# Optimization experiments

Hardware: AMD Instinct MI355X
Metric: run time of the kernel (lower is better)

Reference implementation:

```python
import jax, jax.numpy as jnp
import numpy as np

N_NODES = 20000
N_EDGES = 400000
B = 4            # number of edge_attr tensors in the Python loop (batch of graphs)
NODE_DIM = 256   # == hidden_dim (required: forward feeds raw x into edge_fc)
EDGE_DIM = 16
HIDDEN = 256
OUT_DIM = 128


def setup_inputs() -> dict:
    key = jax.random.key(0)
    ks = jax.random.split(key, 6)
    x = jax.random.normal(ks[0], (N_NODES, NODE_DIM), dtype=jnp.float32)
    edge_index = jax.random.randint(ks[1], (2, N_EDGES), 0, N_NODES, dtype=jnp.int64)
    edge_attrs = jax.random.normal(ks[2], (B, N_EDGES, EDGE_DIM), dtype=jnp.float32)
    fan_in = 2 * HIDDEN + EDGE_DIM  # edge_fc in_features
    W_edge = jax.random.normal(ks[3], (fan_in, HIDDEN), dtype=jnp.float32) / np.sqrt(fan_in).astype(np.float32)
    b_edge = jnp.zeros((HIDDEN,), dtype=jnp.float32)
    W_graph = jax.random.normal(ks[4], (HIDDEN, OUT_DIM), dtype=jnp.float32) / np.sqrt(HIDDEN).astype(np.float32)
    b_graph = jnp.zeros((OUT_DIM,), dtype=jnp.float32)
    return {"x": x, "edge_index": edge_index, "edge_attrs": edge_attrs,
            "W_edge": W_edge, "b_edge": b_edge, "W_graph": W_graph, "b_graph": b_graph}


def reference(x, edge_index, edge_attrs, W_edge, b_edge, W_graph, b_graph):
    # Original: for each edge_attr in edge_attrs:
    #   relu(cat([x[src], x[dst], edge_attr]) @ W_edge + b).mean(0) @ W_graph + b_graph
    # Equivalent: split W_edge by the concat blocks; the (src,dst) contribution is
    # shared across the batch, so compute it once and broadcast.
    D = x.shape[1]
    W_src, W_dst, W_attr = W_edge[:D], W_edge[D:2 * D], W_edge[2 * D:]
    src = x[edge_index[0]]                      # [E, D] gather
    dst = x[edge_index[1]]                      # [E, D] gather
    base = src @ W_src + dst @ W_dst + b_edge   # [E, H]
    h = jax.nn.relu(base[None, :, :] + jnp.einsum('bea,ah->beh', edge_attrs, W_attr))  # [B, E, H]
    graph_feat = h.mean(axis=1)                 # [B, H] mean pool over edges
    return graph_feat @ W_graph + b_graph       # [B, OUT]
```

## Files before the change

kernel.cpp:

```cpp
#include <hip/hip_runtime.h>

#define N_NODES 20000
#define N_EDGES 400000
#define NODE_DIM 256
#define HIDDEN 256
#define OUT_DIM 128
#define PROJ_BLOCKS 628
#define CONV_BLOCKS 256

typedef __attribute__((ext_vector_type(8))) short short8;
typedef __attribute__((ext_vector_type(4))) float f32x4;

__device__ inline unsigned short f2bf(float f) {
  union { float f; unsigned u; } v; v.f = f;
  unsigned r = (v.u + 0x7FFFu + ((v.u >> 16) & 1u)) >> 16;
  return (unsigned short)r;
}

__global__ __launch_bounds__(256) void proj_mfma(
    const float* __restrict__ x, const float* __restrict__ We,
    const float* __restrict__ be, unsigned short* __restrict__ C,
    float* __restrict__ partial, const float* __restrict__ attrs,
    unsigned short* __restrict__ attrs_bf) {
  const int tid = threadIdx.x;
  if (blockIdx.x >= PROJ_BLOCKS) {
    const int nt = CONV_BLOCKS * 256;
    const int total4 = 4 * N_EDGES * 16 / 4;
    for (int i = (blockIdx.x - PROJ_BLOCKS) * 256 + tid; i < total4; i += nt) {
      float4 v = ((const float4*)attrs)[i];
      ushort4 o;
      o.x = f2bf(v.x); o.y = f2bf(v.y); o.z = f2bf(v.z); o.w = f2bf(v.w);
      ((ushort4*)attrs_bf)[i] = o;
    }
    return;
  }
  if (blockIdx.x == 0) {
    for (int i = tid; i < 4 * HIDDEN; i += 256) partial[i] = 0.f;
  }
  const int bm = blockIdx.x >> 2;
  const int bn = blockIdx.x & 3;
  const int row0 = bm * 128;
  const int col0 = bn * 128;
  const int half = col0 >> 8;
  const int ncol0 = col0 & 255;
  const int lane = tid & 63, wave = tid >> 6;
  const int q = lane >> 4, c = lane & 15;
  const int wm = wave >> 1, wn = wave & 1;

  __shared__ unsigned short As[128][32];
  __shared__ unsigned short Bs[128][32];

  f32x4 acc[4][4];
#pragma unroll
  for (int i = 0; i < 4; ++i)
#pragma unroll
    for (int t = 0; t < 4; ++t) acc[i][t] = (f32x4){0.f, 0.f, 0.f, 0.f};

  const int ar = tid >> 1;
  const int ak = (tid & 1) * 16;
  const int bk = tid >> 3;
  const int bn0 = (tid & 7) * 16;

  for (int k0 = 0; k0 < NODE_DIM; k0 += 32) {
    {
      const int r = row0 + ar;
      short8 t0, t1;
      if (r < N_NODES) {
        const float4* src = (const float4*)&x[(size_t)r * NODE_DIM + k0 + ak];
        float4 f0 = src[0], f1 = src[1], f2 = src[2], f3 = src[3];
        t0[0]=f2bf(f0.x); t0[1]=f2bf(f0.y); t0[2]=f2bf(f0.z); t0[3]=f2bf(f0.w);
        t0[4]=f2bf(f1.x); t0[5]=f2bf(f1.y); t0[6]=f2bf(f1.z); t0[7]=f2bf(f1.w);
        t1[0]=f2bf(f2.x); t1[1]=f2bf(f2.y); t1[2]=f2bf(f2.z); t1[3]=f2bf(f2.w);
        t1[4]=f2bf(f3.x); t1[5]=f2bf(f3.y); t1[6]=f2bf(f3.z); t1[7]=f2bf(f3.w);
      } else {
#pragma unroll
        for (int j = 0; j < 8; ++j) { t0[j] = 0; t1[j] = 0; }
      }
      *(short8*)&As[ar][ak] = t0;
      *(short8*)&As[ar][ak + 8] = t1;
    }
    {
      const float4* src = (const float4*)&We[(size_t)(half * 256 + k0 + bk) * HIDDEN + ncol0 + bn0];
#pragma unroll
      for (int v = 0; v < 4; ++v) {
        float4 f = src[v];
        Bs[bn0 + v * 4 + 0][bk] = f2bf(f.x);
        Bs[bn0 + v * 4 + 1][bk] = f2bf(f.y);
        Bs[bn0 + v * 4 + 2][bk] = f2bf(f.z);
        Bs[bn0 + v * 4 + 3][bk] = f2bf(f.w);
      }
    }
    __syncthreads();
    short8 Af[4], Bf[4];
#pragma unroll
    for (int i = 0; i < 4; ++i) Af[i] = *(const short8*)&As[wm * 64 + i * 16 + c][q * 8];
#pragma unroll
    for (int t = 0; t < 4; ++t) Bf[t] = *(const short8*)&Bs[wn * 64 + t * 16 + c][q * 8];
#pragma unroll
    for (int i = 0; i < 4; ++i)
#pragma unroll
      for (int t = 0; t < 4; ++t)
        acc[i][t] = __builtin_amdgcn_mfma_f32_16x16x32_bf16(Af[i], Bf[t], acc[i][t], 0, 0, 0);
    __syncthreads();
  }

  float biasv[4] = {0.f, 0.f, 0.f, 0.f};
  const int nbase = ncol0 + wn * 64;
  if (half) {
#pragma unroll
    for (int t = 0; t < 4; ++t) biasv[t] = be[nbase + t * 16 + c];
  }
#pragma unroll
  for (int i = 0; i < 4; ++i) {
#pragma unroll
    for (int r = 0; r < 4; ++r) {
      const int node = row0 + wm * 64 + i * 16 + q * 4 + r;
      if (node < N_NODES) {
        ushort4 o;
        o.x = f2bf(acc[i][0][r] + biasv[0]);
        o.y = f2bf(acc[i][1][r] + biasv[1]);
        o.z = f2bf(acc[i][2][r] + biasv[2]);
        o.w = f2bf(acc[i][3][r] + biasv[3]);
        *(ushort4*)&C[(size_t)node * 512 + half * 256 + nbase + c * 4] = o;
      }
    }
  }
}

template <bool PRE>
__global__ __launch_bounds__(256) void edge_mfma(
    const unsigned short* __restrict__ C, const int* __restrict__ ei,
    const float* __restrict__ attrs_f, const unsigned short* __restrict__ attrs_b,
    const float* __restrict__ We, float* __restrict__ partial) {
  const int tid = threadIdx.x;
  const int lane = tid & 63, wave = tid >> 6;
  const int q = lane >> 4, c = lane & 15;
  const int hb = wave * 64;

  short8 Bf[4];
#pragma unroll
  for (int t = 0; t < 4; ++t) {
    short8 bf;
#pragma unroll
    for (int j = 0; j < 8; ++j) {
      int k = q * 8 + j;
      float w = (k < 16) ? We[(size_t)(512 + k) * HIDDEN + hb + t * 16 + c] : 0.0f;
      bf[j] = (short)f2bf(w);
    }
    Bf[t] = bf;
  }

  f32x4 acc4[4][4];
#pragma unroll
  for (int b = 0; b < 4; ++b)
#pragma unroll
    for (int t = 0; t < 4; ++t) acc4[b][t] = (f32x4){0.f, 0.f, 0.f, 0.f};

  const f32x4 zero4 = {0.f, 0.f, 0.f, 0.f};
  const int ngroups = N_EDGES / 16;
  for (int g = blockIdx.x; g < ngroups; g += gridDim.x) {
    const int e0 = g * 16;
    const int4 ns4 = *(const int4*)&ei[e0 + q * 4];
    const int4 nd4 = *(const int4*)&ei[N_EDGES + e0 + q * 4];

    short8 Af[4];
    if (PRE) {
      if (q < 2) {
#pragma unroll
        for (int b = 0; b < 4; ++b)
          Af[b] = *(const short8*)&attrs_b[((size_t)b * N_EDGES + e0 + c) * 16 + q * 8];
      } else {
        short8 z;
#pragma unroll
        for (int j = 0; j < 8; ++j) z[j] = 0;
#pragma unroll
        for (int b = 0; b < 4; ++b) Af[b] = z;
      }
    } else {
      if (q < 2) {
#pragma unroll
        for (int b = 0; b < 4; ++b) {
          const size_t off = ((size_t)b * N_EDGES + e0 + c) * 16 + q * 8;
          const float4 a0 = *(const float4*)&attrs_f[off];
          const float4 a1 = *(const float4*)&attrs_f[off + 4];
          short8 af;
          af[0]=f2bf(a0.x); af[1]=f2bf(a0.y); af[2]=f2bf(a0.z); af[3]=f2bf(a0.w);
          af[4]=f2bf(a1.x); af[5]=f2bf(a1.y); af[6]=f2bf(a1.z); af[7]=f2bf(a1.w);
          Af[b] = af;
        }
      } else {
        short8 z;
#pragma unroll
        for (int j = 0; j < 8; ++j) z[j] = 0;
#pragma unroll
        for (int b = 0; b < 4; ++b) Af[b] = z;
      }
    }

    f32x4 base4[4];
    {
      const int nn[4] = {ns4.x, ns4.y, ns4.z, ns4.w};
      const int dd[4] = {nd4.x, nd4.y, nd4.z, nd4.w};
#pragma unroll
      for (int r = 0; r < 4; ++r) {
        const uint2 s = *(const uint2*)&C[(size_t)nn[r] * 512 + hb + c * 4];
        const uint2 d = *(const uint2*)&C[(size_t)dd[r] * 512 + 256 + hb + c * 4];
        base4[0][r] = __uint_as_float(s.x << 16) + __uint_as_float(d.x << 16);
        base4[1][r] = __uint_as_float(s.x & 0xFFFF0000u) + __uint_as_float(d.x & 0xFFFF0000u);
        base4[2][r] = __uint_as_float(s.y << 16) + __uint_as_float(d.y << 16);
        base4[3][r] = __uint_as_float(s.y & 0xFFFF0000u) + __uint_as_float(d.y & 0xFFFF0000u);
      }
    }

#pragma unroll
    for (int b = 0; b < 4; ++b) {
#pragma unroll
      for (int t = 0; t < 4; ++t) {
        f32x4 S = __builtin_amdgcn_mfma_f32_16x16x32_bf16(Af[b], Bf[t], zero4, 0, 0, 0);
        f32x4 u = S + base4[t];
        u[0] = fmaxf(u[0], 0.f); u[1] = fmaxf(u[1], 0.f);
        u[2] = fmaxf(u[2], 0.f); u[3] = fmaxf(u[3], 0.f);
        acc4[b][t] += u;
      }
    }
  }

#pragma unroll
  for (int b = 0; b < 4; ++b)
#pragma unroll
    for (int t = 0; t < 4; ++t) {
      float v = acc4[b][t][0] + acc4[b][t][1] + acc4[b][t][2] + acc4[b][t][3];
      v += __shfl_xor(v, 16, 64);
      v += __shfl_xor(v, 32, 64);
      if (q == 0) atomicAdd(&partial[b * HIDDEN + hb + t * 16 + c], v);
    }
}

__global__ __launch_bounds__(256) void graph_out(
    const float* __restrict__ partial, const float* __restrict__ Wg,
    const float* __restrict__ bg, float* __restrict__ out) {
  const int o = blockIdx.x;
  const int hh = threadIdx.x;
  const int lane = hh & 63, wave = hh >> 6;
  const float w = Wg[(size_t)hh * OUT_DIM + o];
  float v[4];
#pragma unroll
  for (int b = 0; b < 4; ++b) v[b] = partial[b * HIDDEN + hh] * w;
#pragma unroll
  for (int off = 32; off >= 1; off >>= 1)
#pragma unroll
    for (int b = 0; b < 4; ++b) v[b] += __shfl_down(v[b], off, 64);
  __shared__ float red[4][4];
  if (lane == 0)
#pragma unroll
    for (int b = 0; b < 4; ++b) red[wave][b] = v[b];
  __syncthreads();
  if (hh < 4) {
    float s = red[0][hh] + red[1][hh] + red[2][hh] + red[3][hh];
    out[hh * OUT_DIM + o] = s * (1.0f / (float)N_EDGES) + bg[o];
  }
}

extern "C" void kernel_launch(void* const* d_in, const int* in_sizes, int n_in,
                              void* d_out, int out_size, void* d_ws, size_t ws_size,
                              hipStream_t stream) {
  const float* x  = (const float*)d_in[0];
  const int*   ei = (const int*)d_in[1];
  const float* ea = (const float*)d_in[2];
  const float* We = (const float*)d_in[3];
  const float* be = (const float*)d_in[4];
  const float* Wg = (const float*)d_in[5];
  const float* bg = (const float*)d_in[6];
  float* out = (float*)d_out;

  const size_t C_bytes = (size_t)N_NODES * 512 * 2;
  const size_t A_bytes = (size_t)4 * N_EDGES * 16 * 2;
  unsigned short* C = (unsigned short*)d_ws;
  const bool pre = ws_size >= C_bytes + A_bytes + 4096;
  unsigned short* attrs_bf = pre ? (unsigned short*)((char*)d_ws + C_bytes) : nullptr;
  float* partial = (float*)((char*)d_ws + (pre ? C_bytes + A_bytes : C_bytes));

  const int grid1 = pre ? PROJ_BLOCKS + CONV_BLOCKS : PROJ_BLOCKS;
  proj_mfma<<<grid1, 256, 0, stream>>>(x, We, be, C, partial, ea, attrs_bf);
  if (pre)
    edge_mfma<true><<<2048, 256, 0, stream>>>(C, ei, nullptr, attrs_bf, We, partial);
  else
    edge_mfma<false><<<2048, 256, 0, stream>>>(C, ei, ea, nullptr, We, partial);
  graph_out<<<128, 256, 0, stream>>>(partial, Wg, bg, out);
}
```

Measured before the change: 283.7 us.

## Restructure edge kernel around 32x32x16 MFMA with LDS-staged attrs and prefetch

The edge kernel switches from 16x16x32 MFMAs, whose K dimension was half zero-padded, to 32x32x16 MFMAs that use the weight slice as the A operand and the projected base as the accumulator input. To make the gathered row slice line up with the MFMA output layout, the projection kernel now writes columns of C in a permuted order. Attribute tiles are double-buffered into LDS with global_load_lds, and the next group's edge indices are prefetched, with the hidden dimension split across block pairs. This removes wasted MFMA work and the separate base add, and gives wider, contiguous gathers, at the cost of a barrier-based pipeline and a more complex layout coupling between the two kernels.

```diff
diff --git a/kernel.cpp b/kernel.cpp
--- a/kernel.cpp
+++ b/kernel.cpp
@@ -7,15 +7,26 @@
 #define OUT_DIM 128
 #define PROJ_BLOCKS 628
 #define CONV_BLOCKS 256
+#define EDGE_BLOCKS 2048
+#define EG 32
 
 typedef __attribute__((ext_vector_type(8))) short short8;
 typedef __attribute__((ext_vector_type(4))) float f32x4;
+typedef __attribute__((ext_vector_type(16))) float f32x16;
 
 __device__ inline unsigned short f2bf(float f) {
   union { float f; unsigned u; } v; v.f = f;
   unsigned r = (v.u + 0x7FFFu + ((v.u >> 16) & 1u)) >> 16;
   return (unsigned short)r;
 }
+
+__device__ inline void gload_lds16(const void* g, const void* l) {
+  __builtin_amdgcn_global_load_lds(
+      (const __attribute__((address_space(1))) unsigned int*)(unsigned long long)g,
+      (__attribute__((address_space(3))) unsigned int*)(unsigned int)(unsigned long long)l,
+      16, 0, 0);
+}
+
 
 __global__ __launch_bounds__(256) void proj_mfma(
     const float* __restrict__ x, const float* __restrict__ We,
@@ -84,10 +95,14 @@
 #pragma unroll
       for (int v = 0; v < 4; ++v) {
         float4 f = src[v];
-        Bs[bn0 + v * 4 + 0][bk] = f2bf(f.x);
-        Bs[bn0 + v * 4 + 1][bk] = f2bf(f.y);
-        Bs[bn0 + v * 4 + 2][bk] = f2bf(f.z);
-        Bs[bn0 + v * 4 + 3][bk] = f2bf(f.w);
+        const float fv[4] = {f.x, f.y, f.z, f.w};
+#pragma unroll
+        for (int comp = 0; comp < 4; ++comp) {
+          const int wc = bn0 + v * 4 + comp;
+          const int ln = (wc & 64) + (wc & 3) * 16 + ((wc >> 5) & 1) * 8 +
+                         ((wc >> 3) & 3) * 2 + ((wc >> 2) & 1);
+          Bs[ln][bk] = f2bf(fv[comp]);
+        }
       }
     }
     __syncthreads();
@@ -104,11 +119,13 @@
     __syncthreads();
   }
 
+  const int hb1 = c >> 3, q2v = (c >> 1) & 3, chi = c & 1;
+  const int Abase = ncol0 + wn * 64 + hb1 * 32 + chi * 16 + q2v * 4;
+  const int hnat  = ncol0 + wn * 64 + hb1 * 32 + q2v * 8 + chi * 4;
   float biasv[4] = {0.f, 0.f, 0.f, 0.f};
-  const int nbase = ncol0 + wn * 64;
   if (half) {
 #pragma unroll
-    for (int t = 0; t < 4; ++t) biasv[t] = be[nbase + t * 16 + c];
+    for (int t = 0; t < 4; ++t) biasv[t] = be[hnat + t];
   }
 #pragma unroll
   for (int i = 0; i < 4; ++i) {
@@ -121,7 +138,7 @@
         o.y = f2bf(acc[i][1][r] + biasv[1]);
         o.z = f2bf(acc[i][2][r] + biasv[2]);
         o.w = f2bf(acc[i][3][r] + biasv[3]);
-        *(ushort4*)&C[(size_t)node * 512 + half * 256 + nbase + c * 4] = o;
+        *(ushort4*)&C[(size_t)node * 512 + half * 256 + Abase] = o;
       }
     }
   }
@@ -134,106 +151,130 @@
     const float* __restrict__ We, float* __restrict__ partial) {
   const int tid = threadIdx.x;
   const int lane = tid & 63, wave = tid >> 6;
-  const int q = lane >> 4, c = lane & 15;
-  const int hb = wave * 64;
-
-  short8 Bf[4];
-#pragma unroll
-  for (int t = 0; t < 4; ++t) {
-    short8 bf;
-#pragma unroll
-    for (int j = 0; j < 8; ++j) {
-      int k = q * 8 + j;
-      float w = (k < 16) ? We[(size_t)(512 + k) * HIDDEN + hb + t * 16 + c] : 0.0f;
-      bf[j] = (short)f2bf(w);
-    }
-    Bf[t] = bf;
-  }
-
-  f32x4 acc4[4][4];
+  const int le = lane & 31;
+  const int hi = lane >> 5;
+  const int fam = blockIdx.x & 1;
+  const int hblk = fam * 4 + wave;
+  const int hbase = hblk * 32;
+
+  short8 aW;
+#pragma unroll
+  for (int j = 0; j < 8; ++j)
+    aW[j] = (short)f2bf(We[(size_t)(512 + hi * 8 + j) * HIDDEN + hbase + le]);
+
+  f32x16 acc[4];
 #pragma unroll
   for (int b = 0; b < 4; ++b)
 #pragma unroll
-    for (int t = 0; t < 4; ++t) acc4[b][t] = (f32x4){0.f, 0.f, 0.f, 0.f};
-
-  const f32x4 zero4 = {0.f, 0.f, 0.f, 0.f};
-  const int ngroups = N_EDGES / 16;
-  for (int g = blockIdx.x; g < ngroups; g += gridDim.x) {
-    const int e0 = g * 16;
-    const int4 ns4 = *(const int4*)&ei[e0 + q * 4];
-    const int4 nd4 = *(const int4*)&ei[N_EDGES + e0 + q * 4];
-
-    short8 Af[4];
-    if (PRE) {
-      if (q < 2) {
-#pragma unroll
-        for (int b = 0; b < 4; ++b)
-          Af[b] = *(const short8*)&attrs_b[((size_t)b * N_EDGES + e0 + c) * 16 + q * 8];
-      } else {
-        short8 z;
-#pragma unroll
-        for (int j = 0; j < 8; ++j) z[j] = 0;
-#pragma unroll
-        for (int b = 0; b < 4; ++b) Af[b] = z;
-      }
+    for (int r = 0; r < 16; ++r) acc[b][r] = 0.f;
+
+  __shared__ unsigned short attr_s[2][4][512];
+  const size_t sgoff = (size_t)(le * 16 + hi * 8);
+
+  const int ngroups = N_EDGES / EG;
+  const int stride = gridDim.x >> 1;
+  const int g0 = blockIdx.x >> 1;
+
+  int buf = 0;
+  int ns, nd;
+  {
+    if constexpr (PRE) {
+      const unsigned short* gp =
+          attrs_b + ((size_t)wave * N_EDGES + (size_t)g0 * EG) * 16 + sgoff;
+      gload_lds16(gp, &attr_s[0][wave][0]);
+    }
+    ns = ei[g0 * EG + le];
+    nd = ei[N_EDGES + g0 * EG + le];
+  }
+
+  for (int g = g0; g < ngroups; g += stride) {
+    const int gn = g + stride;
+    const int gsafe = (gn < ngroups) ? gn : g;
+
+    const size_t so = (size_t)ns * 512 + hbase + hi * 16;
+    const size_t dofs = (size_t)nd * 512 + 256 + hbase + hi * 16;
+    const uint4 s0 = *(const uint4*)(C + so);
+    const uint4 s1 = *(const uint4*)(C + so + 8);
+    const uint4 d0 = *(const uint4*)(C + dofs);
+    const uint4 d1 = *(const uint4*)(C + dofs + 8);
+    const int ns2 = ei[gsafe * EG + le];
+    const int nd2 = ei[N_EDGES + gsafe * EG + le];
+
+    short8 Bb[4];
+    if constexpr (PRE) {
+      asm volatile("s_waitcnt vmcnt(6)" ::: "memory");
+      __builtin_amdgcn_s_barrier();
+      {
+        const unsigned short* gp =
+            attrs_b + ((size_t)wave * N_EDGES + (size_t)gsafe * EG) * 16 + sgoff;
+        gload_lds16(gp, &attr_s[buf ^ 1][wave][0]);
+      }
+#pragma unroll
+      for (int b = 0; b < 4; ++b)
+        Bb[b] = *(const short8*)&attr_s[buf][b][(size_t)lane * 8];
     } else {
-      if (q < 2) {
-#pragma unroll
-        for (int b = 0; b < 4; ++b) {
-          const size_t off = ((size_t)b * N_EDGES + e0 + c) * 16 + q * 8;
-          const float4 a0 = *(const float4*)&attrs_f[off];
-          const float4 a1 = *(const float4*)&attrs_f[off + 4];
-          short8 af;
-          af[0]=f2bf(a0.x); af[1]=f2bf(a0.y); af[2]=f2bf(a0.z); af[3]=f2bf(a0.w);
-          af[4]=f2bf(a1.x); af[5]=f2bf(a1.y); af[6]=f2bf(a1.z); af[7]=f2bf(a1.w);
-          Af[b] = af;
-        }
-      } else {
-        short8 z;
-#pragma unroll
-        for (int j = 0; j < 8; ++j) z[j] = 0;
-#pragma unroll
-        for (int b = 0; b < 4; ++b) Af[b] = z;
-      }
-    }
-
-    f32x4 base4[4];
-    {
-      const int nn[4] = {ns4.x, ns4.y, ns4.z, ns4.w};
-      const int dd[4] = {nd4.x, nd4.y, nd4.z, nd4.w};
-#pragma unroll
-      for (int r = 0; r < 4; ++r) {
-        const uint2 s = *(const uint2*)&C[(size_t)nn[r] * 512 + hb + c * 4];
-        const uint2 d = *(const uint2*)&C[(size_t)dd[r] * 512 + 256 + hb + c * 4];
-        base4[0][r] = __uint_as_float(s.x << 16) + __uint_as_float(d.x << 16);
-        base4[1][r] = __uint_as_float(s.x & 0xFFFF0000u) + __uint_as_float(d.x & 0xFFFF0000u);
-        base4[2][r] = __uint_as_float(s.y << 16) + __uint_as_float(d.y << 16);
-        base4[3][r] = __uint_as_float(s.y & 0xFFFF0000u) + __uint_as_float(d.y & 0xFFFF0000u);
-      }
-    }
+#pragma unroll
+      for (int b = 0; b < 4; ++b) {
+        const size_t aoff =
+            ((size_t)b * N_EDGES + (size_t)g * EG + le) * 16 + hi * 8;
+        const float4 a0 = *(const float4*)(attrs_f + aoff);
+        const float4 a1 = *(const float4*)(attrs_f + aoff + 4);
+        short8 bb;
+        bb[0]=f2bf(a0.x); bb[1]=f2bf(a0.y); bb[2]=f2bf(a0.z); bb[3]=f2bf(a0.w);
+        bb[4]=f2bf(a1.x); bb[5]=f2bf(a1.y); bb[6]=f2bf(a1.z); bb[7]=f2bf(a1.w);
+        Bb[b] = bb;
+      }
+    }
+
+    f32x16 base;
+    base[0]  = __uint_as_float(s0.x << 16)        + __uint_as_float(d0.x << 16);
+    base[1]  = __uint_as_float(s0.x & 0xFFFF0000u) + __uint_as_float(d0.x & 0xFFFF0000u);
+    base[2]  = __uint_as_float(s0.y << 16)        + __uint_as_float(d0.y << 16);
+    base[3]  = __uint_as_float(s0.y & 0xFFFF0000u) + __uint_as_float(d0.y & 0xFFFF0000u);
+    base[4]  = __uint_as_float(s0.z << 16)        + __uint_as_float(d0.z << 16);
+    base[5]  = __uint_as_float(s0.z & 0xFFFF0000u) + __uint_as_float(d0.z & 0xFFFF0000u);
+    base[6]  = __uint_as_float(s0.w << 16)        + __uint_as_float(d0.w << 16);
+    base[7]  = __uint_as_float(s0.w & 0xFFFF0000u) + __uint_as_float(d0.w & 0xFFFF0000u);
+    base[8]  = __uint_as_float(s1.x << 16)        + __uint_as_float(d1.x << 16);
+    base[9]  = __uint_as_float(s1.x & 0xFFFF0000u) + __uint_as_float(d1.x & 0xFFFF0000u);
+    base[10] = __uint_as_float(s1.y << 16)        + __uint_as_float(d1.y << 16);
+    base[11] = __uint_as_float(s1.y & 0xFFFF0000u) + __uint_as_float(d1.y & 0xFFFF0000u);
+    base[12] = __uint_as_float(s1.z << 16)        + __uint_as_float(d1.z << 16);
+    base[13] = __uint_as_float(s1.z & 0xFFFF0000u) + __uint_as_float(d1.z & 0xFFFF0000u);
+    base[14] = __uint_as_float(s1.w << 16)        + __uint_as_float(d1.w << 16);
+    base[15] = __uint_as_float(s1.w & 0xFFFF0000u) + __uint_as_float(d1.w & 0xFFFF0000u);
 
 #pragma unroll
     for (int b = 0; b < 4; ++b) {
-#pragma unroll
-      for (int t = 0; t < 4; ++t) {
-        f32x4 S = __builtin_amdgcn_mfma_f32_16x16x32_bf16(Af[b], Bf[t], zero4, 0, 0, 0);
-        f32x4 u = S + base4[t];
-        u[0] = fmaxf(u[0], 0.f); u[1] = fmaxf(u[1], 0.f);
-        u[2] = fmaxf(u[2], 0.f); u[3] = fmaxf(u[3], 0.f);
-        acc4[b][t] += u;
-      }
-    }
+      f32x16 S = __builtin_amdgcn_mfma_f32_32x32x16_bf16(aW, Bb[b], base, 0, 0, 0);
+#pragma unroll
+      for (int r = 0; r < 16; ++r) acc[b][r] += fmaxf(S[r], 0.f);
+    }
+
+    ns = ns2; nd = nd2; buf ^= 1;
   }
 
 #pragma unroll
   for (int b = 0; b < 4; ++b)
 #pragma unroll
-    for (int t = 0; t < 4; ++t) {
-      float v = acc4[b][t][0] + acc4[b][t][1] + acc4[b][t][2] + acc4[b][t][3];
+    for (int r = 0; r < 16; ++r) {
+      float v = acc[b][r];
+      v += __shfl_xor(v, 1, 64);
+      v += __shfl_xor(v, 2, 64);
+      v += __shfl_xor(v, 4, 64);
+      v += __shfl_xor(v, 8, 64);
       v += __shfl_xor(v, 16, 64);
-      v += __shfl_xor(v, 32, 64);
-      if (q == 0) atomicAdd(&partial[b * HIDDEN + hb + t * 16 + c], v);
-    }
+      acc[b][r] = v;
+    }
+  if (le == 0) {
+#pragma unroll
+    for (int b = 0; b < 4; ++b)
+#pragma unroll
+      for (int r = 0; r < 16; ++r) {
+        const int h = hbase + (r & 3) + 8 * (r >> 2) + 4 * hi;
+        atomicAdd(&partial[b * HIDDEN + h], acc[b][r]);
+      }
+  }
 }
 
 __global__ __launch_bounds__(256) void graph_out(
@@ -283,8 +324,8 @@
   const int grid1 = pre ? PROJ_BLOCKS + CONV_BLOCKS : PROJ_BLOCKS;
   proj_mfma<<<grid1, 256, 0, stream>>>(x, We, be, C, partial, ea, attrs_bf);
   if (pre)
-    edge_mfma<true><<<2048, 256, 0, stream>>>(C, ei, nullptr, attrs_bf, We, partial);
+    edge_mfma<true><<<EDGE_BLOCKS, 256, 0, stream>>>(C, ei, nullptr, attrs_bf, We, partial);
   else
-    edge_mfma<false><<<2048, 256, 0, stream>>>(C, ei, ea, nullptr, We, partial);
+    edge_mfma<false><<<EDGE_BLOCKS, 256, 0, stream>>>(C, ei, ea, nullptr, We, partial);
   graph_out<<<128, 256, 0, stream>>>(partial, Wg, bg, out);
 }
```

Measured after the change: 437.7 us. 1.54x slower.

## Pre-convert x and W to bf16 and use LDS-direct loads in projection GEMM

Applied to the files above, without the earlier changes.

Adds a prep kernel that converts x, edge attributes and a transposed W_edge to bf16 in workspace and zeroes the partial sums. A new projection kernel loads bf16 tiles straight into LDS with global_load_lds and runs MFMA on them, replacing the fp32-reading projection. This tier runs only when the workspace is large enough. It adds an extra launch plus an extra pass over x to save conversion work and fp32 traffic inside the GEMM. The new GEMM does not double-buffer and syncs twice per k-step.

```diff
diff --git a/kernel.cpp b/kernel.cpp
--- a/kernel.cpp
+++ b/kernel.cpp
@@ -15,6 +15,125 @@
   union { float f; unsigned u; } v; v.f = f;
   unsigned r = (v.u + 0x7FFFu + ((v.u >> 16) & 1u)) >> 16;
   return (unsigned short)r;
+}
+
+__device__ inline void gload_lds16(const void* g, const void* l) {
+  __builtin_amdgcn_global_load_lds(
+      (const __attribute__((address_space(1))) unsigned int*)(unsigned long long)g,
+      (__attribute__((address_space(3))) unsigned int*)(unsigned int)(unsigned long long)l,
+      16, 0, 0);
+}
+
+__global__ __launch_bounds__(256) void prep(
+    const float* __restrict__ x, const float* __restrict__ We,
+    const float* __restrict__ attrs, unsigned short* __restrict__ xb,
+    unsigned short* __restrict__ Wt, unsigned short* __restrict__ ab,
+    float* __restrict__ partial) {
+  const int tid = threadIdx.x;
+  const int gtid = blockIdx.x * 256 + tid;
+  const int nt = gridDim.x * 256;
+  if (blockIdx.x == 0) {
+    for (int i = tid; i < 4 * HIDDEN; i += 256) partial[i] = 0.f;
+  }
+  const int x4 = N_NODES * NODE_DIM / 4;
+  const int a4 = 4 * N_EDGES * 16 / 4;
+  for (int i = gtid; i < x4 + a4; i += nt) {
+    float4 v;
+    unsigned short* dst;
+    if (i < x4) {
+      v = ((const float4*)x)[i];
+      dst = xb + (size_t)i * 4;
+    } else {
+      v = ((const float4*)attrs)[i - x4];
+      dst = ab + (size_t)(i - x4) * 4;
+    }
+    ushort4 o;
+    o.x = f2bf(v.x); o.y = f2bf(v.y); o.z = f2bf(v.z); o.w = f2bf(v.w);
+    *(ushort4*)dst = o;
+  }
+  for (int i = gtid; i < 2 * 256 * 64; i += nt) {
+    const int row = i >> 6;
+    const int k4 = (i & 63) * 4;
+    const int half = row >> 8, n = row & 255;
+    ushort4 o;
+    o.x = f2bf(We[(size_t)(half * 256 + k4 + 0) * HIDDEN + n]);
+    o.y = f2bf(We[(size_t)(half * 256 + k4 + 1) * HIDDEN + n]);
+    o.z = f2bf(We[(size_t)(half * 256 + k4 + 2) * HIDDEN + n]);
+    o.w = f2bf(We[(size_t)(half * 256 + k4 + 3) * HIDDEN + n]);
+    *(ushort4*)&Wt[(size_t)row * 256 + k4] = o;
+  }
+}
+
+__global__ __launch_bounds__(256) void proj_bf(
+    const unsigned short* __restrict__ xb, const unsigned short* __restrict__ Wt,
+    const float* __restrict__ be, unsigned short* __restrict__ C) {
+  const int tid = threadIdx.x;
+  const int bm = blockIdx.x >> 2;
+  const int bn = blockIdx.x & 3;
+  const int row0 = bm * 128;
+  const int col0 = bn * 128;
+  const int half = col0 >> 8;
+  const int ncol0 = col0 & 255;
+  const int lane = tid & 63, wave = tid >> 6;
+  const int q = lane >> 4, c = lane & 15;
+  const int wm = wave >> 1, wn = wave & 1;
+
+  __shared__ unsigned short As[128][32];
+  __shared__ unsigned short Bs[128][32];
+
+  f32x4 acc[4][4];
+#pragma unroll
+  for (int i = 0; i < 4; ++i)
+#pragma unroll
+    for (int t = 0; t < 4; ++t) acc[i][t] = (f32x4){0.f, 0.f, 0.f, 0.f};
+
+  const int sm = wave * 16 + (lane >> 2);
+  const int skc = (lane & 3) * 8;
+  int ra0 = row0 + sm;       if (ra0 >= N_NODES) ra0 = 0;
+  int ra1 = row0 + 64 + sm;  if (ra1 >= N_NODES) ra1 = 0;
+  const int nb0 = half * 256 + ncol0 + sm;
+  const int nb1 = nb0 + 64;
+
+  for (int k0 = 0; k0 < NODE_DIM; k0 += 32) {
+    gload_lds16(xb + (size_t)ra0 * 256 + k0 + skc, &As[wave * 16][0]);
+    gload_lds16(xb + (size_t)ra1 * 256 + k0 + skc, &As[64 + wave * 16][0]);
+    gload_lds16(Wt + (size_t)nb0 * 256 + k0 + skc, &Bs[wave * 16][0]);
+    gload_lds16(Wt + (size_t)nb1 * 256 + k0 + skc, &Bs[64 + wave * 16][0]);
+    __syncthreads();
+    short8 Af[4], Bf[4];
+#pragma unroll
+    for (int i = 0; i < 4; ++i) Af[i] = *(const short8*)&As[wm * 64 + i * 16 + c][q * 8];
+#pragma unroll
+    for (int t = 0; t < 4; ++t) Bf[t] = *(const short8*)&Bs[wn * 64 + t * 16 + c][q * 8];
+#pragma unroll
+    for (int i = 0; i < 4; ++i)
+#pragma unroll
+      for (int t = 0; t < 4; ++t)
+        acc[i][t] = __builtin_amdgcn_mfma_f32_16x16x32_bf16(Af[i], Bf[t], acc[i][t], 0, 0, 0);
+    __syncthreads();
+  }
+
+  float biasv[4] = {0.f, 0.f, 0.f, 0.f};
+  const int nbase = ncol0 + wn * 64;
+  if (half) {
+#pragma unroll
+    for (int t = 0; t < 4; ++t) biasv[t] = be[nbase + t * 16 + c];
+  }
+#pragma unroll
+  for (int i = 0; i < 4; ++i) {
+#pragma unroll
+    for (int r = 0; r < 4; ++r) {
+      const int node = row0 + wm * 64 + i * 16 + q * 4 + r;
+      if (node < N_NODES) {
+        ushort4 o;
+        o.x = f2bf(acc[i][0][r] + biasv[0]);
+        o.y = f2bf(acc[i][1][r] + biasv[1]);
+        o.z = f2bf(acc[i][2][r] + biasv[2]);
+        o.w = f2bf(acc[i][3][r] + biasv[3]);
+        *(ushort4*)&C[(size_t)node * 512 + half * 256 + nbase + c * 4] = o;
+      }
+    }
+  }
 }
 
 __global__ __launch_bounds__(256) void proj_mfma(
@@ -275,16 +394,32 @@
 
   const size_t C_bytes = (size_t)N_NODES * 512 * 2;
   const size_t A_bytes = (size_t)4 * N_EDGES * 16 * 2;
+  const size_t X_bytes = (size_t)N_NODES * NODE_DIM * 2;
+  const size_t W_bytes = (size_t)2 * 256 * 256 * 2;
   unsigned short* C = (unsigned short*)d_ws;
-  const bool pre = ws_size >= C_bytes + A_bytes + 4096;
-  unsigned short* attrs_bf = pre ? (unsigned short*)((char*)d_ws + C_bytes) : nullptr;
-  float* partial = (float*)((char*)d_ws + (pre ? C_bytes + A_bytes : C_bytes));
-
-  const int grid1 = pre ? PROJ_BLOCKS + CONV_BLOCKS : PROJ_BLOCKS;
-  proj_mfma<<<grid1, 256, 0, stream>>>(x, We, be, C, partial, ea, attrs_bf);
-  if (pre)
+
+  const bool tier2 = ws_size >= C_bytes + A_bytes + X_bytes + W_bytes + 4096;
+  const bool tier1 = ws_size >= C_bytes + A_bytes + 4096;
+
+  if (tier2) {
+    unsigned short* attrs_bf = (unsigned short*)((char*)d_ws + C_bytes);
+    unsigned short* xb = (unsigned short*)((char*)d_ws + C_bytes + A_bytes);
+    unsigned short* Wt = (unsigned short*)((char*)d_ws + C_bytes + A_bytes + X_bytes);
+    float* partial = (float*)((char*)d_ws + C_bytes + A_bytes + X_bytes + W_bytes);
+    prep<<<2048, 256, 0, stream>>>(x, We, ea, xb, Wt, attrs_bf, partial);
+    proj_bf<<<PROJ_BLOCKS, 256, 0, stream>>>(xb, Wt, be, C);
     edge_mfma<true><<<2048, 256, 0, stream>>>(C, ei, nullptr, attrs_bf, We, partial);
-  else
+    graph_out<<<128, 256, 0, stream>>>(partial, Wg, bg, out);
+  } else if (tier1) {
+    unsigned short* attrs_bf = (unsigned short*)((char*)d_ws + C_bytes);
+    float* partial = (float*)((char*)d_ws + C_bytes + A_bytes);
+    proj_mfma<<<PROJ_BLOCKS + CONV_BLOCKS, 256, 0, stream>>>(x, We, be, C, partial, ea, attrs_bf);
+    edge_mfma<true><<<2048, 256, 0, stream>>>(C, ei, nullptr, attrs_bf, We, partial);
+    graph_out<<<128, 256, 0, stream>>>(partial, Wg, bg, out);
+  } else {
+    float* partial = (float*)((char*)d_ws + C_bytes);
+    proj_mfma<<<PROJ_BLOCKS, 256, 0, stream>>>(x, We, be, C, partial, ea, nullptr);
     edge_mfma<false><<<2048, 256, 0, stream>>>(C, ei, ea, nullptr, We, partial);
-  graph_out<<<128, 256, 0, stream>>>(partial, Wg, bg, out);
-}
+    graph_out<<<128, 256, 0, stream>>>(partial, Wg, bg, out);
+  }
+}
```

New measurement: 287.2 us. No clear change (+1.2%).
